# Performance work log

Measured on AMD Instinct MI355X. Metric: run time of the kernel, lower is better.

## Reference

```python
import jax, jax.numpy as jnp
import numpy as np

WH, WW = 7, 7
NUM_HEADS = 8

def _relative_position_index(Wh, Ww):
    coords = np.stack(np.meshgrid(np.arange(Wh), np.arange(Ww), indexing='ij'))  # (2, Wh, Ww)
    cf = coords.reshape(2, -1)                       # (2, N)
    rc = cf[:, :, None] - cf[:, None, :]             # (2, N, N)
    rc = rc.transpose(1, 2, 0).astype(np.int64)      # (N, N, 2)
    rc[..., 0] += Wh - 1
    rc[..., 1] += Ww - 1
    rc[..., 0] *= 2 * Ww - 1
    return rc.sum(-1)                                # (N, N)

_REL_IDX = jnp.asarray(_relative_position_index(WH, WW))


def setup_inputs() -> dict:
    key = jax.random.key(0)
    ks = jax.random.split(key, 9)
    B_, N, C = 2048, 49, 256
    nW = 64
    return {
        'x': jax.random.normal(ks[0], (B_, N, C), jnp.float32),
        'mask': jax.random.normal(ks[1], (nW, N, N), jnp.float32),
        'sal_fg_attn_mask': jax.random.normal(ks[2], (B_, N, N), jnp.float32),
        'sal_bg_attn_mask': jax.random.normal(ks[3], (B_, N, N), jnp.float32),
        'qkv_w': jax.random.normal(ks[4], (3 * C, C), jnp.float32) * 0.02,
        'qkv_b': jax.random.normal(ks[5], (3 * C,), jnp.float32) * 0.02,
        'proj_w': jax.random.normal(ks[6], (C, C), jnp.float32) * 0.02,
        'proj_b': jax.random.normal(ks[7], (C,), jnp.float32) * 0.02,
        'rel_pos_bias_table': jax.random.normal(ks[8], ((2 * WH - 1) * (2 * WW - 1), NUM_HEADS), jnp.float32) * 0.02,
    }


def reference(x, mask, sal_fg_attn_mask, sal_bg_attn_mask, qkv_w, qkv_b, proj_w, proj_b, rel_pos_bias_table):
    B_, N, C = x.shape
    H = NUM_HEADS
    hd = C // H
    scale = hd ** -0.5

    qkv = x @ qkv_w.T + qkv_b                        # (B_, N, 3C)
    qkv = qkv.reshape(B_, N, 3, H, hd).transpose(2, 0, 3, 1, 4)  # (3, B_, H, N, hd)
    q, k, v = qkv[0] * scale, qkv[1], qkv[2]

    attn = jnp.einsum('bhqd,bhkd->bhqk', q, k)       # (B_, H, N, N)
    bias = rel_pos_bias_table[_REL_IDX]              # (N, N, H)
    attn = attn + bias.transpose(2, 0, 1)[None]      # broadcast over B_

    attn_fg = attn + sal_fg_attn_mask[:, None]
    attn_bg = attn + sal_bg_attn_mask[:, None]

    nW = mask.shape[0]
    m = mask[None, :, None]                          # (1, nW, 1, N, N)

    def masked_softmax(a):
        a = a.reshape(B_ // nW, nW, H, N, N) + m
        return jax.nn.softmax(a.reshape(B_, H, N, N), axis=-1)

    attn = masked_softmax(attn)
    attn_fg = masked_softmax(attn_fg)
    attn_bg = masked_softmax(attn_bg)

    def av(a):
        return jnp.einsum('bhqk,bhkd->bqhd', a, v).reshape(B_, N, C)

    out = av(attn) + av(attn_fg) - av(attn_bg)
    return out @ proj_w.T + proj_b
```

## Files before the change

kernel.cpp:

```cpp
#include <hip/hip_runtime.h>
#include <hip/hip_bf16.h>
#include <math.h>


#define B_TOT   2048
#define NTOK    49
#define CDIM    256
#define NHEAD   8
#define HDIM    32
#define MROWS   (B_TOT * NTOK)
#define QKV_N   (3 * CDIM)

#define LOG2E 1.4426950408889634f

#if __has_builtin(__builtin_amdgcn_exp2f)
#define EXP2(x) __builtin_amdgcn_exp2f(x)
#else
#define EXP2(x) __expf((x) * 0.6931471805599453f)
#endif

typedef __attribute__((ext_vector_type(8))) short short8;
typedef __attribute__((ext_vector_type(4))) float floatx4;

typedef unsigned int u32_g __attribute__((address_space(1)));
typedef unsigned int u32_l __attribute__((address_space(3)));

__device__ __forceinline__ void gld_lds16(const void* g, void* l) {
    __builtin_amdgcn_global_load_lds((const u32_g*)g, (u32_l*)l, 16, 0, 0);
}

__global__ __launch_bounds__(256) void cast_kernel(
    const float* __restrict__ in, __hip_bfloat16* __restrict__ out, int n8)
{
    const int i = blockIdx.x * 256 + threadIdx.x;
    if (i >= n8) return;
    const float4* p = (const float4*)in + (size_t)i * 2;
    float4 a = p[0], b = p[1];
    __hip_bfloat16 r[8];
    r[0] = __float2bfloat16(a.x); r[1] = __float2bfloat16(a.y);
    r[2] = __float2bfloat16(a.z); r[3] = __float2bfloat16(a.w);
    r[4] = __float2bfloat16(b.x); r[5] = __float2bfloat16(b.y);
    r[6] = __float2bfloat16(b.z); r[7] = __float2bfloat16(b.w);
    *(uint4*)(out + (size_t)i * 8) = *(const uint4*)r;
}

__global__ __launch_bounds__(256) void prep_wmask(
    const float* __restrict__ wmask,
    const float* __restrict__ table,
    float* __restrict__ wmp)
{
    const int idx = blockIdx.x * 256 + threadIdx.x;
    const int col = idx & 63, row = (idx >> 6) & 63;
    const int h = (idx >> 12) & 7, win = idx >> 15;
    float v = -1e30f;
    if (row < 49 && col < 49) {
        const int qi = row / 7, qj = row % 7;
        const int ki = col / 7, kj = col % 7;
        const int ti = (qi - ki + 6) * 13 + (qj - kj + 6);
        v = (wmask[win * 2401 + row * 49 + col] + table[ti * 8 + h]) * LOG2E;
    }
    wmp[idx] = v;
}

__global__ __launch_bounds__(256) void prep_expmask(
    const float* __restrict__ in, float* __restrict__ out)
{
    const int i = blockIdx.x * 256 + threadIdx.x;
    float4 a = ((const float4*)in)[i];
    float4 r;
    r.x = EXP2(a.x * LOG2E); r.y = EXP2(a.y * LOG2E);
    r.z = EXP2(a.z * LOG2E); r.w = EXP2(a.w * LOG2E);
    ((float4*)out)[i] = r;
}

template<int NDIM, bool OUT_BF16>
__global__ __launch_bounds__(256) void gemm_mfma(
    const __hip_bfloat16* __restrict__ A,
    const __hip_bfloat16* __restrict__ W,
    const float* __restrict__ bias,
    void* __restrict__ Yv)
{
    const int K = 256;
    __shared__ short As[128 * 64];
    __shared__ short Bs[128 * 64];
    const int t = threadIdx.x;
    const int lane = t & 63, w = t >> 6;
    const int wr = w >> 1, wc = w & 1;
    const int q = lane >> 4, l15 = lane & 15;

    constexpr int NBX = NDIM / 128;
    constexpr int NWG = NBX * (MROWS / 128);
    int bid = blockIdx.y * NBX + blockIdx.x;
    bid = (bid & 7) * (NWG >> 3) + (bid >> 3);
    const int m0 = (bid / NBX) * 128, n0 = (bid % NBX) * 128;

    const int srow = t >> 3, skb = t & 7;
    const int gkb = skb ^ (srow & 7);
    const __hip_bfloat16* Ag = A + (size_t)(m0 + srow) * K + gkb * 8;
    const __hip_bfloat16* Wg = W + (size_t)(n0 + srow) * K + gkb * 8;

    floatx4 acc[4][4] = {};
    const int swz = l15 & 7;

    for (int k0 = 0; k0 < K; k0 += 64) {
        __syncthreads();
        #pragma unroll
        for (int i = 0; i < 4; i++) {
            gld_lds16(Ag + (size_t)(i * 32) * K + k0, &As[i * 2048 + w * 512]);
            gld_lds16(Wg + (size_t)(i * 32) * K + k0, &Bs[i * 2048 + w * 512]);
        }
        __syncthreads();
        #pragma unroll
        for (int kk = 0; kk < 2; kk++) {
            const int kbs = ((kk << 2) + q) ^ swz;
            short8 af[4], bf[4];
            #pragma unroll
            for (int i = 0; i < 4; i++) {
                af[i] = *(const short8*)&As[(wr * 64 + i * 16 + l15) * 64 + kbs * 8];
                bf[i] = *(const short8*)&Bs[(wc * 64 + i * 16 + l15) * 64 + kbs * 8];
            }
            #pragma unroll
            for (int i = 0; i < 4; i++)
                #pragma unroll
                for (int j = 0; j < 4; j++)
                    acc[i][j] = __builtin_amdgcn_mfma_f32_16x16x32_bf16(
                        af[i], bf[j], acc[i][j], 0, 0, 0);
        }
    }

    #pragma unroll
    for (int j = 0; j < 4; j++) {
        const int n = n0 + wc * 64 + j * 16 + l15;
        const float bv = bias[n];
        #pragma unroll
        for (int i = 0; i < 4; i++) {
            #pragma unroll
            for (int r = 0; r < 4; r++) {
                const int m = m0 + wr * 64 + i * 16 + q * 4 + r;
                const float val = acc[i][j][r] + bv;
                if (OUT_BF16)
                    ((__hip_bfloat16*)Yv)[(size_t)m * NDIM + n] = __float2bfloat16(val);
                else
                    ((float*)Yv)[(size_t)m * NDIM + n] = val;
            }
        }
    }
}

__global__ __launch_bounds__(256, 4) void attn_kernel(
    const __hip_bfloat16* __restrict__ Y,
    const float* __restrict__ wmp,
    const float* __restrict__ Fgp,
    const float* __restrict__ Bgp,
    __hip_bfloat16* __restrict__ O)
{
    __shared__ __hip_bfloat16 sQ[64 * 40];
    __shared__ __hip_bfloat16 sK[64 * 40];
    __shared__ __hip_bfloat16 sVt[32 * 72];
    __shared__ __hip_bfloat16 sP[64 * 72];

    const int blk = blockIdx.x;
    const int b = (blk >> 6) * 8 + (blk & 7);
    const int h = (blk >> 3) & 7;
    const int t = threadIdx.x;
    const int w = t >> 6, lane = t & 63;
    const int quad = lane >> 4, l15 = lane & 15;
    const float SC = 0.17677669529663687f * LOG2E;

    const float* wmb = wmp + (((size_t)(b & 63) * 8 + h) << 12);
    const float* fgb = Fgp + (size_t)b * (NTOK * NTOK);
    const float* bgb = Bgp + (size_t)b * (NTOK * NTOK);
    float mwm[16], mfg[16], mbg[16];
    #pragma unroll
    for (int r = 0; r < 4; r++) {
        const int row = w * 16 + quad * 4 + r;
        const int rc49 = min(row, 48) * 49;
        const float* pw = wmb + row * 64 + l15;
        const float* pf = fgb + rc49 + l15;
        const float* pb = bgb + rc49 + l15;
        mwm[r * 4 + 0] = pw[0];  mwm[r * 4 + 1] = pw[16];
        mwm[r * 4 + 2] = pw[32]; mwm[r * 4 + 3] = pw[48];
        mfg[r * 4 + 0] = pf[0];  mfg[r * 4 + 1] = pf[16];
        mfg[r * 4 + 2] = pf[32]; mfg[r * 4 + 3] = fgb[rc49 + 48];
        mbg[r * 4 + 0] = pb[0];  mbg[r * 4 + 1] = pb[16];
        mbg[r * 4 + 2] = pb[32]; mbg[r * 4 + 3] = bgb[rc49 + 48];
    }
    const __hip_bfloat16* Yb = Y + (size_t)b * NTOK * QKV_N + h * HDIM;
    if (t < 196) {
        const int n = t >> 2, c = t & 3;
        uint4 qv = *(const uint4*)(Yb + (size_t)n * QKV_N + c * 8);
        uint4 kv = *(const uint4*)(Yb + (size_t)n * QKV_N + 256 + c * 8);
        uint4 vv = *(const uint4*)(Yb + (size_t)n * QKV_N + 512 + c * 8);
        *(uint4*)(sQ + n * 40 + c * 8) = qv;
        *(uint4*)(sK + n * 40 + c * 8) = kv;
        const __hip_bfloat16* vp = (const __hip_bfloat16*)&vv;
        #pragma unroll
        for (int j = 0; j < 8; j++)
            sVt[(c * 8 + j) * 72 + n] = vp[j];
    }
    {
        unsigned int* pK = (unsigned int*)sK;
        #pragma unroll
        for (int i = 980 + t; i < 1280; i += 256) pK[i] = 0u;
    }
    {
        const __hip_bfloat16 z = __float2bfloat16(0.f);
        #pragma unroll
        for (int it = 0; it < 2; it++) {
            const int idx = t + it * 256;
            const int d = idx >> 4, c = 49 + (idx & 15);
            sVt[d * 72 + c] = z;
        }
    }
    __syncthreads();

    floatx4 acc[4];
    {
        short8 af = *(const short8*)(sQ + (w * 16 + l15) * 40 + quad * 8);
        #pragma unroll
        for (int nt = 0; nt < 4; nt++) {
            short8 bf = *(const short8*)(sK + (nt * 16 + l15) * 40 + quad * 8);
            floatx4 z = {};
            acc[nt] = __builtin_amdgcn_mfma_f32_16x16x32_bf16(af, bf, z, 0, 0, 0);
        }
    }

    float e0[16];
    #pragma unroll
    for (int r = 0; r < 4; r++)
        #pragma unroll
        for (int nt = 0; nt < 4; nt++)
            e0[r * 4 + nt] = EXP2(fmaf(acc[nt][r], SC, mwm[r * 4 + nt]));
    #pragma unroll
    for (int i = 0; i < 16; i++) mfg[i] *= e0[i];
    #pragma unroll
    for (int i = 0; i < 16; i++) mbg[i] *= e0[i];

    float s0[4], sf[4], sb[4];
    #pragma unroll
    for (int r = 0; r < 4; r++) {
        s0[r] = (e0[r * 4] + e0[r * 4 + 1]) + (e0[r * 4 + 2] + e0[r * 4 + 3]);
        sf[r] = (mfg[r * 4] + mfg[r * 4 + 1]) + (mfg[r * 4 + 2] + mfg[r * 4 + 3]);
        sb[r] = (mbg[r * 4] + mbg[r * 4 + 1]) + (mbg[r * 4 + 2] + mbg[r * 4 + 3]);
    }
    #pragma unroll
    for (int st = 1; st < 16; st <<= 1)
        #pragma unroll
        for (int r = 0; r < 4; r++) {
            s0[r] += __shfl_xor(s0[r], st);
            sf[r] += __shfl_xor(sf[r], st);
            sb[r] += __shfl_xor(sb[r], st);
        }

    float pc[16];
    #pragma unroll
    for (int r = 0; r < 4; r++) {
        const float r0 = __builtin_amdgcn_rcpf(s0[r]);
        const float rf = __builtin_amdgcn_rcpf(sf[r]);
        const float rb = -__builtin_amdgcn_rcpf(sb[r]);
        #pragma unroll
        for (int nt = 0; nt < 4; nt++) {
            const int i = r * 4 + nt;
            pc[i] = fmaf(mbg[i], rb, fmaf(mfg[i], rf, e0[i] * r0));
        }
    }

    #pragma unroll
    for (int r = 0; r < 4; r++) {
        const int row = w * 16 + quad * 4 + r;
        #pragma unroll
        for (int nt = 0; nt < 4; nt++)
            sP[row * 72 + nt * 16 + l15] = __float2bfloat16(pc[r * 4 + nt]);
    }
    __syncthreads();

    floatx4 o0 = {}, o1 = {};
    {
        short8 a0  = *(const short8*)(sP + (w * 16 + l15) * 72 + quad * 8);
        short8 a1  = *(const short8*)(sP + (w * 16 + l15) * 72 + 32 + quad * 8);
        short8 b00 = *(const short8*)(sVt + l15 * 72 + quad * 8);
        short8 b01 = *(const short8*)(sVt + l15 * 72 + 32 + quad * 8);
        short8 b10 = *(const short8*)(sVt + (16 + l15) * 72 + quad * 8);
        short8 b11 = *(const short8*)(sVt + (16 + l15) * 72 + 32 + quad * 8);
        o0 = __builtin_amdgcn_mfma_f32_16x16x32_bf16(a0, b00, o0, 0, 0, 0);
        o0 = __builtin_amdgcn_mfma_f32_16x16x32_bf16(a1, b01, o0, 0, 0, 0);
        o1 = __builtin_amdgcn_mfma_f32_16x16x32_bf16(a0, b10, o1, 0, 0, 0);
        o1 = __builtin_amdgcn_mfma_f32_16x16x32_bf16(a1, b11, o1, 0, 0, 0);
    }
    __hip_bfloat16* Ob = O + (size_t)b * NTOK * CDIM + h * HDIM;
    #pragma unroll
    for (int r = 0; r < 4; r++) {
        const int m = w * 16 + quad * 4 + r;
        if (m < NTOK) {
            Ob[(size_t)m * CDIM + l15]      = __float2bfloat16(o0[r]);
            Ob[(size_t)m * CDIM + 16 + l15] = __float2bfloat16(o1[r]);
        }
    }
}

extern "C" void kernel_launch(void* const* d_in, const int* in_sizes, int n_in,
                              void* d_out, int out_size, void* d_ws, size_t ws_size,
                              hipStream_t stream) {
    const float* x      = (const float*)d_in[0];
    const float* mask   = (const float*)d_in[1];
    const float* fg     = (const float*)d_in[2];
    const float* bg     = (const float*)d_in[3];
    const float* qkv_w  = (const float*)d_in[4];
    const float* qkv_b  = (const float*)d_in[5];
    const float* proj_w = (const float*)d_in[6];
    const float* proj_b = (const float*)d_in[7];
    const float* table  = (const float*)d_in[8];
    float* out = (float*)d_out;

    char* ws = (char*)d_ws;
    __hip_bfloat16* xb  = (__hip_bfloat16*)(ws);
    __hip_bfloat16* Ybf = (__hip_bfloat16*)(ws + 51380224);
    __hip_bfloat16* Obf = (__hip_bfloat16*)(ws + 205520896);
    __hip_bfloat16* qwb = (__hip_bfloat16*)(ws + 256901120);
    __hip_bfloat16* pwb = (__hip_bfloat16*)(ws + 257294336);
    float* wmp = (float*)(ws);
    float* Fgp = (float*)(ws + 8388608);
    float* Bgp = (float*)(ws + 28057600);

    dim3 blk(256);
    cast_kernel<<<dim3((MROWS * CDIM / 8 + 255) / 256), blk, 0, stream>>>(x, xb, MROWS * CDIM / 8);
    cast_kernel<<<dim3((QKV_N * CDIM / 8 + 255) / 256), blk, 0, stream>>>(qkv_w, qwb, QKV_N * CDIM / 8);
    cast_kernel<<<dim3((CDIM * CDIM / 8 + 255) / 256), blk, 0, stream>>>(proj_w, pwb, CDIM * CDIM / 8);

    gemm_mfma<QKV_N, true><<<dim3(QKV_N / 128, MROWS / 128), blk, 0, stream>>>(xb, qwb, qkv_b, Ybf);

    prep_wmask<<<dim3(8192), blk, 0, stream>>>(mask, table, wmp);
    prep_expmask<<<dim3(4802), blk, 0, stream>>>(fg, Fgp);
    prep_expmask<<<dim3(4802), blk, 0, stream>>>(bg, Bgp);

    attn_kernel<<<dim3(B_TOT * NHEAD), blk, 0, stream>>>(Ybf, wmp, Fgp, Bgp, Obf);
    gemm_mfma<CDIM, false><<<dim3(CDIM / 128, MROWS / 128), blk, 0, stream>>>(Obf, pwb, proj_b, out);
}
```

Measured before the change: 396.4 us.

## Fuse input cast into QKV GEMM with register prefetch and vectorized epilogue

After: 586.2 us. +47.9%, slower.

```diff
diff --git a/kernel.cpp b/kernel.cpp
--- a/kernel.cpp
+++ b/kernel.cpp
@@ -21,13 +21,6 @@
 
 typedef __attribute__((ext_vector_type(8))) short short8;
 typedef __attribute__((ext_vector_type(4))) float floatx4;
-
-typedef unsigned int u32_g __attribute__((address_space(1)));
-typedef unsigned int u32_l __attribute__((address_space(3)));
-
-__device__ __forceinline__ void gld_lds16(const void* g, void* l) {
-    __builtin_amdgcn_global_load_lds((const u32_g*)g, (u32_l*)l, 16, 0, 0);
-}
 
 __global__ __launch_bounds__(256) void cast_kernel(
     const float* __restrict__ in, __hip_bfloat16* __restrict__ out, int n8)
@@ -73,9 +66,9 @@
     ((float4*)out)[i] = r;
 }
 
-template<int NDIM, bool OUT_BF16>
+template<int NDIM, bool OUT_BF16, bool A_FP32>
 __global__ __launch_bounds__(256) void gemm_mfma(
-    const __hip_bfloat16* __restrict__ A,
+    const void* __restrict__ Av,
     const __hip_bfloat16* __restrict__ W,
     const float* __restrict__ bias,
     void* __restrict__ Yv)
@@ -96,19 +89,49 @@
 
     const int srow = t >> 3, skb = t & 7;
     const int gkb = skb ^ (srow & 7);
-    const __hip_bfloat16* Ag = A + (size_t)(m0 + srow) * K + gkb * 8;
+    const float* A32 = (const float*)Av;
+    const __hip_bfloat16* A16 = (const __hip_bfloat16*)Av;
     const __hip_bfloat16* Wg = W + (size_t)(n0 + srow) * K + gkb * 8;
+
+    float4 ar32[4][2];
+    uint4  ar16[4];
+    uint4  wrg[4];
+
+    auto load_tile = [&](int k0) {
+        #pragma unroll
+        for (int i = 0; i < 4; i++) {
+            if (A_FP32) {
+                const float* p = A32 + (size_t)(m0 + i * 32 + srow) * K + gkb * 8 + k0;
+                ar32[i][0] = *(const float4*)p;
+                ar32[i][1] = *(const float4*)(p + 4);
+            } else {
+                ar16[i] = *(const uint4*)(A16 + (size_t)(m0 + i * 32 + srow) * K + gkb * 8 + k0);
+            }
+            wrg[i] = *(const uint4*)(Wg + (size_t)(i * 32) * K + k0);
+        }
+    };
 
     floatx4 acc[4][4] = {};
     const int swz = l15 & 7;
 
+    load_tile(0);
+    #pragma unroll
     for (int k0 = 0; k0 < K; k0 += 64) {
         __syncthreads();
         #pragma unroll
         for (int i = 0; i < 4; i++) {
-            gld_lds16(Ag + (size_t)(i * 32) * K + k0, &As[i * 2048 + w * 512]);
-            gld_lds16(Wg + (size_t)(i * 32) * K + k0, &Bs[i * 2048 + w * 512]);
-        }
+            if (A_FP32) {
+                const float* f = (const float*)&ar32[i][0];
+                __hip_bfloat16 tmp[8];
+                #pragma unroll
+                for (int e = 0; e < 8; e++) tmp[e] = __float2bfloat16(f[e]);
+                *(uint4*)&As[i * 2048 + t * 8] = *(const uint4*)tmp;
+            } else {
+                *(uint4*)&As[i * 2048 + t * 8] = ar16[i];
+            }
+            *(uint4*)&Bs[i * 2048 + t * 8] = wrg[i];
+        }
+        if (k0 + 64 < K) load_tile(k0 + 64);
         __syncthreads();
         #pragma unroll
         for (int kk = 0; kk < 2; kk++) {
@@ -124,30 +147,37 @@
                 #pragma unroll
                 for (int j = 0; j < 4; j++)
                     acc[i][j] = __builtin_amdgcn_mfma_f32_16x16x32_bf16(
-                        af[i], bf[j], acc[i][j], 0, 0, 0);
-        }
-    }
-
-    #pragma unroll
-    for (int j = 0; j < 4; j++) {
-        const int n = n0 + wc * 64 + j * 16 + l15;
-        const float bv = bias[n];
-        #pragma unroll
-        for (int i = 0; i < 4; i++) {
-            #pragma unroll
-            for (int r = 0; r < 4; r++) {
-                const int m = m0 + wr * 64 + i * 16 + q * 4 + r;
-                const float val = acc[i][j][r] + bv;
-                if (OUT_BF16)
-                    ((__hip_bfloat16*)Yv)[(size_t)m * NDIM + n] = __float2bfloat16(val);
-                else
-                    ((float*)Yv)[(size_t)m * NDIM + n] = val;
+                        bf[j], af[i], acc[i][j], 0, 0, 0);
+        }
+    }
+
+    float4 bv[4];
+    #pragma unroll
+    for (int j = 0; j < 4; j++)
+        bv[j] = *(const float4*)&bias[n0 + wc * 64 + j * 16 + q * 4];
+    #pragma unroll
+    for (int i = 0; i < 4; i++) {
+        const size_t mrow = (size_t)(m0 + wr * 64 + i * 16 + l15) * NDIM;
+        #pragma unroll
+        for (int j = 0; j < 4; j++) {
+            const int n = n0 + wc * 64 + j * 16 + q * 4;
+            const float v0 = acc[i][j][0] + bv[j].x;
+            const float v1 = acc[i][j][1] + bv[j].y;
+            const float v2 = acc[i][j][2] + bv[j].z;
+            const float v3 = acc[i][j][3] + bv[j].w;
+            if (OUT_BF16) {
+                __hip_bfloat16 o[4] = {__float2bfloat16(v0), __float2bfloat16(v1),
+                                       __float2bfloat16(v2), __float2bfloat16(v3)};
+                *(uint2*)((__hip_bfloat16*)Yv + mrow + n) = *(const uint2*)o;
+            } else {
+                float4 o = {v0, v1, v2, v3};
+                *(float4*)((float*)Yv + mrow + n) = o;
             }
         }
     }
 }
 
-__global__ __launch_bounds__(256, 4) void attn_kernel(
+__global__ __launch_bounds__(256, 6) void attn_kernel(
     const __hip_bfloat16* __restrict__ Y,
     const float* __restrict__ wmp,
     const float* __restrict__ Fgp,
@@ -313,7 +343,6 @@
     float* out = (float*)d_out;
 
     char* ws = (char*)d_ws;
-    __hip_bfloat16* xb  = (__hip_bfloat16*)(ws);
     __hip_bfloat16* Ybf = (__hip_bfloat16*)(ws + 51380224);
     __hip_bfloat16* Obf = (__hip_bfloat16*)(ws + 205520896);
     __hip_bfloat16* qwb = (__hip_bfloat16*)(ws + 256901120);
@@ -323,16 +352,13 @@
     float* Bgp = (float*)(ws + 28057600);
 
     dim3 blk(256);
-    cast_kernel<<<dim3((MROWS * CDIM / 8 + 255) / 256), blk, 0, stream>>>(x, xb, MROWS * CDIM / 8);
     cast_kernel<<<dim3((QKV_N * CDIM / 8 + 255) / 256), blk, 0, stream>>>(qkv_w, qwb, QKV_N * CDIM / 8);
     cast_kernel<<<dim3((CDIM * CDIM / 8 + 255) / 256), blk, 0, stream>>>(proj_w, pwb, CDIM * CDIM / 8);
-
-    gemm_mfma<QKV_N, true><<<dim3(QKV_N / 128, MROWS / 128), blk, 0, stream>>>(xb, qwb, qkv_b, Ybf);
-
     prep_wmask<<<dim3(8192), blk, 0, stream>>>(mask, table, wmp);
     prep_expmask<<<dim3(4802), blk, 0, stream>>>(fg, Fgp);
     prep_expmask<<<dim3(4802), blk, 0, stream>>>(bg, Bgp);
 
+    gemm_mfma<QKV_N, true, true><<<dim3(QKV_N / 128, MROWS / 128), blk, 0, stream>>>(x, qwb, qkv_b, Ybf);
     attn_kernel<<<dim3(B_TOT * NHEAD), blk, 0, stream>>>(Ybf, wmp, Fgp, Bgp, Obf);
-    gemm_mfma<CDIM, false><<<dim3(CDIM / 128, MROWS / 128), blk, 0, stream>>>(Obf, pwb, proj_b, out);
-}
+    gemm_mfma<CDIM, false, false><<<dim3(CDIM / 128, MROWS / 128), blk, 0, stream>>>(Obf, pwb, proj_b, out);
+}
```
